# Kernel tuning notes

Hardware: AMD Instinct MI355X
Metric: run time of the kernel (lower is better)

## Reference

```python
import jax, jax.numpy as jnp
import numpy as np

ALPHA = 0.5
SMOOTH = 1e-05
ITERS = 10


def _max_pool3x3(x):
    # 3x3 max pool, stride 1, SAME padding on NCHW tensor
    return jax.lax.reduce_window(
        x, -jnp.inf, jax.lax.max,
        window_dimensions=(1, 1, 3, 3),
        window_strides=(1, 1, 1, 1),
        padding='SAME')


def _soft_erode(x):
    return -_max_pool3x3(-x)


def _soft_dilate(x):
    return _max_pool3x3(x)


def _soft_skeletonize(img, iterations=ITERS):
    def body(skel, _):
        eroded = _soft_erode(skel)
        temp = _soft_dilate(eroded)
        skel = skel - (skel - eroded) * temp
        skel = jnp.clip(skel, 0.0, 1.0)
        return skel, None
    skel, _ = jax.lax.scan(body, img, None, length=iterations)
    return skel


def _dice_score(pred, target, smooth=SMOOTH):
    inter = jnp.sum(pred * target, axis=(2, 3))
    union = jnp.sum(pred, axis=(2, 3)) + jnp.sum(target, axis=(2, 3))
    dice = (2.0 * inter + smooth) / (union + smooth)
    return jnp.mean(dice)


def setup_inputs() -> dict:
    key = jax.random.key(0)
    k1, k2 = jax.random.split(key)
    B, C, H, W = 32, 1, 512, 512
    pred_logits = jax.random.normal(k1, (B, C, H, W), dtype=jnp.float32)
    target = jax.random.uniform(k2, (B, C, H, W), dtype=jnp.float32)
    return {"pred_logits": pred_logits, "target": target}


def reference(pred_logits, target):
    pred = jax.nn.sigmoid(pred_logits)
    dice = _dice_score(pred, target)
    pred_skel = _soft_skeletonize(pred)
    target_skel = _soft_skeletonize(target)
    skel_dice = _dice_score(pred_skel, target_skel)
    loss = (1.0 - ALPHA) * (1.0 - dice) + ALPHA * (1.0 - skel_dice)
    return (loss, dice, skel_dice)
```

## Files before the change

### kernel.cpp

```cpp
#include <hip/hip_runtime.h>
#include <hip/hip_fp16.h>
#include <math.h>


#define H 512
#define W 512
#define IMG (H * W)
#define NIMG 64
#define NPRED 32

#define APU 72
#define AROWS 74
#define BPU 68
#define BROWS 68
#define TQ 17
#define S1ITEMS 238
#define FILLN (AROWS * 18)

#define PINF2 0x7C007C00u
#define NINF2 0xFC00FC00u
#define ONE2  0x3C003C00u

typedef _Float16 f16;
typedef _Float16 h2 __attribute__((ext_vector_type(2)));
typedef __fp16 fp16v2 __attribute__((ext_vector_type(2)));

__device__ __forceinline__ float2 unpack2(uint u) {
    fp16v2 h = __builtin_bit_cast(fp16v2, u);
    return make_float2((float)h.x, (float)h.y);
}
__device__ __forceinline__ uint pack2(float a, float b) {
    fp16v2 h = __builtin_amdgcn_cvt_pkrtz(a, b);
    return __builtin_bit_cast(uint, h);
}
__device__ __forceinline__ uint pmin(uint a, uint b) {
    uint d; asm("v_pk_min_f16 %0, %1, %2" : "=v"(d) : "v"(a), "v"(b)); return d;
}
__device__ __forceinline__ uint pmax(uint a, uint b) {
    uint d; asm("v_pk_max_f16 %0, %1, %2" : "=v"(d) : "v"(a), "v"(b)); return d;
}
__device__ __forceinline__ uint abit(uint hi, uint lo) {
    return __builtin_amdgcn_alignbit(hi, lo, 16);
}

__device__ __forceinline__ float wsum64(float v) {
#pragma unroll
    for (int o = 32; o > 0; o >>= 1) v += __shfl_down(v, o);
    return v;
}

__device__ __forceinline__ void hmin8p(const uint* __restrict__ p, uint m[6], uint sc[4]) {
    uint4 w0 = *(const uint4*)(p);
    uint4 w1 = *(const uint4*)(p + 4);
    uint w[8] = {w0.x, w0.y, w0.z, w0.w, w1.x, w1.y, w1.z, w1.w};
    sc[0] = w[2]; sc[1] = w[3]; sc[2] = w[4]; sc[3] = w[5];
    uint s[7];
#pragma unroll
    for (int j = 0; j < 7; j++) s[j] = abit(w[j + 1], w[j]);
#pragma unroll
    for (int i = 0; i < 6; i++) m[i] = pmin(s[i], pmin(w[i + 1], s[i + 1]));
}

template<bool EDGE>
__device__ __forceinline__ void erode8(const uint a[6], const uint b[6], const uint c[6],
                                       bool rowok, const bool* eok, uint e[6]) {
#pragma unroll
    for (int i = 0; i < 6; i++) {
        uint v = pmin(a[i], pmin(b[i], c[i]));
        e[i] = EDGE ? ((rowok && eok[i]) ? v : NINF2) : v;
    }
}

__device__ __forceinline__ void hmax8(const uint e[6], uint hx[4], uint ec[4]) {
    uint a[5];
#pragma unroll
    for (int j = 0; j < 5; j++) a[j] = abit(e[j + 1], e[j]);
#pragma unroll
    for (int p = 0; p < 4; p++) {
        hx[p] = pmax(a[p], pmax(e[p + 1], a[p + 1]));
        ec[p] = e[p + 1];
    }
}

__device__ __forceinline__ uint upd_pair(uint s, uint ec, uint t) {
    h2 sh = __builtin_bit_cast(h2, s);
    h2 eh = __builtin_bit_cast(h2, ec);
    h2 th = __builtin_bit_cast(h2, t);
    h2 o = sh - (sh - eh) * th;
    return pmin(pmax(__builtin_bit_cast(uint, o), 0u), ONE2);
}

template<bool EDGE, int SIG>
__device__ float2 fillA_f32(uint* __restrict__ A, const float* __restrict__ src,
                            const float* __restrict__ tgt,
                            int tileX, int tileY, int tid) {
    float a = 0.0f, b = 0.0f;
    for (int i = tid; i < FILLN; i += 256) {
        const int r = i / 18;
        const int q = i - 18 * r;
        const int gy = tileY + r - 4;
        const int gx = tileX - 8 + 8 * q;
        uint4 v = make_uint4(PINF2, PINF2, PINF2, PINF2);
        const bool ok = EDGE ? (r < 72 && (unsigned)gy < (unsigned)H &&
                                (unsigned)gx < (unsigned)W)
                             : true;
        if (ok) {
            const float* sp = src + (size_t)gy * W + gx;
            float4 f0 = *(const float4*)(sp);
            float4 f1 = *(const float4*)(sp + 4);
            if (SIG) {
                f0.x = 1.0f / (1.0f + __expf(-f0.x));
                f0.y = 1.0f / (1.0f + __expf(-f0.y));
                f0.z = 1.0f / (1.0f + __expf(-f0.z));
                f0.w = 1.0f / (1.0f + __expf(-f0.w));
                f1.x = 1.0f / (1.0f + __expf(-f1.x));
                f1.y = 1.0f / (1.0f + __expf(-f1.y));
                f1.z = 1.0f / (1.0f + __expf(-f1.z));
                f1.w = 1.0f / (1.0f + __expf(-f1.w));
            }
            if (((unsigned)(r - 4) < 64u) && ((unsigned)(q - 1) < 16u)) {
                if (SIG) {
                    const float* tp = tgt + (size_t)gy * W + gx;
                    float4 t0 = *(const float4*)(tp);
                    float4 t1 = *(const float4*)(tp + 4);
                    a += f0.x * t0.x + f0.y * t0.y + f0.z * t0.z + f0.w * t0.w
                       + f1.x * t1.x + f1.y * t1.y + f1.z * t1.z + f1.w * t1.w;
                    b += f0.x + f0.y + f0.z + f0.w + f1.x + f1.y + f1.z + f1.w;
                } else {
                    a += f0.x + f0.y + f0.z + f0.w + f1.x + f1.y + f1.z + f1.w;
                }
            }
            v.x = pack2(f0.x, f0.y); v.y = pack2(f0.z, f0.w);
            v.z = pack2(f1.x, f1.y); v.w = pack2(f1.z, f1.w);
        }
        *(uint4*)(A + r * APU + 4 * q) = v;
    }
    return make_float2(a, b);
}

template<bool EDGE>
__device__ void fillA_f16(uint* __restrict__ A, const f16* __restrict__ src,
                          int tileX, int tileY, int tid) {
    for (int i = tid; i < FILLN; i += 256) {
        const int r = i / 18;
        const int q = i - 18 * r;
        const int gy = tileY + r - 4;
        const int gx = tileX - 8 + 8 * q;
        uint4 v;
        if (EDGE) {
            v = make_uint4(PINF2, PINF2, PINF2, PINF2);
            if (r < 72 && (unsigned)gy < (unsigned)H && (unsigned)gx < (unsigned)W)
                v = *(const uint4*)(src + (size_t)gy * W + gx);
        } else {
            v = *(const uint4*)(src + (size_t)gy * W + gx);
        }
        *(uint4*)(A + r * APU + 4 * q) = v;
    }
}

template<bool EDGE>
__device__ void stage1(const uint* __restrict__ Au, uint* __restrict__ Bu,
                       int tileX, int tileY, int tid) {
    if (tid >= S1ITEMS) return;
    const int s = tid / TQ;
    const int g = tid - TQ * s;
    const int gcb = tileX + 8 * g - 4;
    const int ys = tileY - 2 + 5 * s;
    bool eok[6], wok[4];
    if (EDGE) {
#pragma unroll
        for (int i = 0; i < 6; i++) eok[i] = ((unsigned)(gcb - 2 + 2 * i) < (unsigned)W);
#pragma unroll
        for (int p = 0; p < 4; p++) wok[p] = ((unsigned)(gcb + 2 * p) < (unsigned)W);
    }
    const int lr = 5 * s + 2;
    const uint* Ab = Au + 4 * g;
    uint m[3][6], sc[3][4], hx[3][4], e[6], ec_cur[4], ec_nxt[4], tsc[4];
    hmin8p(Ab + (lr - 2) * APU, m[0], tsc);
    hmin8p(Ab + (lr - 1) * APU, m[1], tsc);
    hmin8p(Ab + (lr + 0) * APU, m[2], sc[0]);
    erode8<EDGE>(m[0], m[1], m[2], (unsigned)(ys - 1) < (unsigned)H, eok, e);
    hmax8(e, hx[0], ec_nxt);
    hmin8p(Ab + (lr + 1) * APU, m[0], sc[1]);
    erode8<EDGE>(m[1], m[2], m[0], (unsigned)ys < (unsigned)H, eok, e);
    hmax8(e, hx[1], ec_cur);
#pragma unroll
    for (int k = 0; k < 5; k++) {
        hmin8p(Ab + (lr + 2 + k) * APU, m[(k + 1) % 3], sc[(2 + k) % 3]);
        erode8<EDGE>(m[(k + 2) % 3], m[k % 3], m[(k + 1) % 3],
                     (unsigned)(ys + k + 1) < (unsigned)H, eok, e);
        hmax8(e, hx[(k + 2) % 3], ec_nxt);
        const int br = 5 * s + k;
        if (br < BROWS) {
            const bool rin = EDGE ? ((unsigned)(ys + k) < (unsigned)H) : true;
            uint o[4];
#pragma unroll
            for (int p = 0; p < 4; p++) {
                uint t = pmax(hx[k % 3][p], pmax(hx[(k + 1) % 3][p], hx[(k + 2) % 3][p]));
                uint v = upd_pair(sc[k % 3][p], ec_cur[p], t);
                o[p] = EDGE ? ((rin && wok[p]) ? v : PINF2) : v;
            }
            *(uint4*)(Bu + br * BPU + 4 * g) = make_uint4(o[0], o[1], o[2], o[3]);
        }
#pragma unroll
        for (int p = 0; p < 4; p++) ec_cur[p] = ec_nxt[p];
    }
}

template<bool EDGE, bool TOREG>
__device__ void stage2(const uint* __restrict__ Bu, int tileX, int tileY, int tid,
                       f16* __restrict__ gdst, uint* __restrict__ oreg) {
    const int g = tid & 15;
    const int ty = tid >> 4;
    const int X = tileX + 8 * g;
    const int gy0 = tileY + 4 * ty;
    const int rb = 4 * ty + 2;
    bool eok[6];
    if (EDGE) {
#pragma unroll
        for (int i = 0; i < 6; i++) eok[i] = ((unsigned)(X - 2 + 2 * i) < (unsigned)W);
    }
    const uint* Bb = Bu + 4 * g;
    uint m[3][6], sc[3][4], hx[3][4], e[6], ec_cur[4], ec_nxt[4], tsc[4];
    hmin8p(Bb + (rb - 2) * BPU, m[0], tsc);
    hmin8p(Bb + (rb - 1) * BPU, m[1], tsc);
    hmin8p(Bb + (rb + 0) * BPU, m[2], sc[0]);
    erode8<EDGE>(m[0], m[1], m[2], (unsigned)(gy0 - 1) < (unsigned)H, eok, e);
    hmax8(e, hx[0], ec_nxt);
    hmin8p(Bb + (rb + 1) * BPU, m[0], sc[1]);
    erode8<EDGE>(m[1], m[2], m[0], true, eok, e);
    hmax8(e, hx[1], ec_cur);
#pragma unroll
    for (int k = 0; k < 4; k++) {
        hmin8p(Bb + (rb + 2 + k) * BPU, m[(k + 1) % 3], sc[(2 + k) % 3]);
        erode8<EDGE>(m[(k + 2) % 3], m[k % 3], m[(k + 1) % 3],
                     (unsigned)(gy0 + k + 1) < (unsigned)H, eok, e);
        hmax8(e, hx[(k + 2) % 3], ec_nxt);
        uint o[4];
#pragma unroll
        for (int p = 0; p < 4; p++) {
            uint t = pmax(hx[k % 3][p], pmax(hx[(k + 1) % 3][p], hx[(k + 2) % 3][p]));
            o[p] = upd_pair(sc[k % 3][p], ec_cur[p], t);
        }
        if (TOREG) {
#pragma unroll
            for (int p = 0; p < 4; p++) oreg[4 * k + p] = o[p];
        } else {
            *(uint4*)(gdst + (size_t)(gy0 + k) * W + X) = make_uint4(o[0], o[1], o[2], o[3]);
        }
#pragma unroll
        for (int p = 0; p < 4; p++) ec_cur[p] = ec_nxt[p];
    }
}

__device__ __forceinline__ bool is_edge() {
    return (blockIdx.x == 0) | (blockIdx.x == 3) | (blockIdx.y == 0) | (blockIdx.y == 7);
}

__global__ __launch_bounds__(256, 4) void k_first(
    const float* __restrict__ logits, const float* __restrict__ target,
    f16* __restrict__ outb, float* __restrict__ parts0, float* __restrict__ parts1) {
    __shared__ __align__(16) uint A[AROWS * APU];
    __shared__ __align__(16) uint Bu[BROWS * BPU];
    __shared__ float red[8];
    const int img = blockIdx.z;
    const int tileX = blockIdx.x * 128, tileY = blockIdx.y * 64;
    const int tid = threadIdx.x;
    const bool pred = (img < NPRED);
    const bool edge = is_edge();
    float2 ab;
    if (edge) {
        if (pred) ab = fillA_f32<true, 1>(A, logits + (size_t)img * IMG,
                                          target + (size_t)img * IMG, tileX, tileY, tid);
        else      ab = fillA_f32<true, 0>(A, target + (size_t)(img - NPRED) * IMG,
                                          nullptr, tileX, tileY, tid);
    } else {
        if (pred) ab = fillA_f32<false, 1>(A, logits + (size_t)img * IMG,
                                           target + (size_t)img * IMG, tileX, tileY, tid);
        else      ab = fillA_f32<false, 0>(A, target + (size_t)(img - NPRED) * IMG,
                                           nullptr, tileX, tileY, tid);
    }
    __syncthreads();
    float a = wsum64(ab.x), b = wsum64(ab.y);
    if ((tid & 63) == 0) { red[tid >> 6] = a; red[4 + (tid >> 6)] = b; }
    if (edge) stage1<true>(A, Bu, tileX, tileY, tid);
    else      stage1<false>(A, Bu, tileX, tileY, tid);
    __syncthreads();
    if (tid == 0) {
        int bi = blockIdx.z * 32 + blockIdx.y * 4 + blockIdx.x;
        parts0[bi] = red[0] + red[1] + red[2] + red[3];
        parts1[bi] = red[4] + red[5] + red[6] + red[7];
    }
    if (edge) stage2<true, false>(Bu, tileX, tileY, tid, outb + (size_t)img * IMG, nullptr);
    else      stage2<false, false>(Bu, tileX, tileY, tid, outb + (size_t)img * IMG, nullptr);
}

__global__ __launch_bounds__(256, 4) void k_mid(
    const f16* __restrict__ in, f16* __restrict__ outb) {
    __shared__ __align__(16) uint A[AROWS * APU];
    __shared__ __align__(16) uint Bu[BROWS * BPU];
    const int img = blockIdx.z;
    const int tileX = blockIdx.x * 128, tileY = blockIdx.y * 64;
    const int tid = threadIdx.x;
    const bool edge = is_edge();
    if (edge) {
        fillA_f16<true>(A, in + (size_t)img * IMG, tileX, tileY, tid);
        __syncthreads();
        stage1<true>(A, Bu, tileX, tileY, tid);
        __syncthreads();
        stage2<true, false>(Bu, tileX, tileY, tid, outb + (size_t)img * IMG, nullptr);
    } else {
        fillA_f16<false>(A, in + (size_t)img * IMG, tileX, tileY, tid);
        __syncthreads();
        stage1<false>(A, Bu, tileX, tileY, tid);
        __syncthreads();
        stage2<false, false>(Bu, tileX, tileY, tid, outb + (size_t)img * IMG, nullptr);
    }
}

__global__ __launch_bounds__(256, 4) void k_last(
    const f16* __restrict__ in, float* __restrict__ pA,
    float* __restrict__ pB, float* __restrict__ pC) {
    __shared__ __align__(16) uint A[AROWS * APU];
    __shared__ __align__(16) uint Bu[BROWS * BPU];
    __shared__ float red[12];
    const int img = blockIdx.z;
    const int tileX = blockIdx.x * 128, tileY = blockIdx.y * 64;
    const int tid = threadIdx.x;
    const bool edge = is_edge();
    uint op[16], ot[16];
    if (edge) {
        fillA_f16<true>(A, in + (size_t)img * IMG, tileX, tileY, tid);
        __syncthreads();
        stage1<true>(A, Bu, tileX, tileY, tid);
        __syncthreads();
        stage2<true, true>(Bu, tileX, tileY, tid, nullptr, op);
        fillA_f16<true>(A, in + (size_t)(img + NPRED) * IMG, tileX, tileY, tid);
        __syncthreads();
        stage1<true>(A, Bu, tileX, tileY, tid);
        __syncthreads();
        stage2<true, true>(Bu, tileX, tileY, tid, nullptr, ot);
    } else {
        fillA_f16<false>(A, in + (size_t)img * IMG, tileX, tileY, tid);
        __syncthreads();
        stage1<false>(A, Bu, tileX, tileY, tid);
        __syncthreads();
        stage2<false, true>(Bu, tileX, tileY, tid, nullptr, op);
        fillA_f16<false>(A, in + (size_t)(img + NPRED) * IMG, tileX, tileY, tid);
        __syncthreads();
        stage1<false>(A, Bu, tileX, tileY, tid);
        __syncthreads();
        stage2<false, true>(Bu, tileX, tileY, tid, nullptr, ot);
    }
    float a = 0.0f, b = 0.0f, c = 0.0f;
#pragma unroll
    for (int j = 0; j < 16; j++) {
        float2 p = unpack2(op[j]);
        float2 t = unpack2(ot[j]);
        a += p.x * t.x + p.y * t.y;
        b += p.x + p.y;
        c += t.x + t.y;
    }
    a = wsum64(a); b = wsum64(b); c = wsum64(c);
    if ((tid & 63) == 0) {
        red[tid >> 6] = a; red[4 + (tid >> 6)] = b; red[8 + (tid >> 6)] = c;
    }
    __syncthreads();
    if (tid == 0) {
        int bi = img * 32 + blockIdx.y * 4 + blockIdx.x;
        pA[bi] = red[0] + red[1] + red[2] + red[3];
        pB[bi] = red[4] + red[5] + red[6] + red[7];
        pC[bi] = red[8] + red[9] + red[10] + red[11];
    }
}

__global__ __launch_bounds__(64) void finalize_img(
    const float* __restrict__ parts0, const float* __restrict__ parts1,
    const float* __restrict__ pA, const float* __restrict__ pB,
    const float* __restrict__ pC, float* __restrict__ dices) {
    const int i = blockIdx.x, t = threadIdx.x;
    const bool v = (t < 32);
    float inter = wsum64(v ? parts0[i * 32 + t] : 0.0f);
    float sp = wsum64(v ? parts1[i * 32 + t] : 0.0f);
    float st = wsum64(v ? parts0[(NPRED + i) * 32 + t] : 0.0f);
    float i2 = wsum64(v ? pA[i * 32 + t] : 0.0f);
    float sp2 = wsum64(v ? pB[i * 32 + t] : 0.0f);
    float st2 = wsum64(v ? pC[i * 32 + t] : 0.0f);
    if (t == 0) {
        dices[i] = (float)((2.0 * (double)inter + 1e-5) / ((double)sp + (double)st + 1e-5));
        dices[32 + i] = (float)((2.0 * (double)i2 + 1e-5) / ((double)sp2 + (double)st2 + 1e-5));
    }
}

__global__ void finalize_out(const float* __restrict__ dices, float* __restrict__ out) {
    const int t = threadIdx.x;
    double d = 0.0, sd = 0.0;
    if (t < 32) { d = dices[t]; sd = dices[32 + t]; }
#pragma unroll
    for (int o = 32; o > 0; o >>= 1) { d += __shfl_down(d, o); sd += __shfl_down(sd, o); }
    if (t == 0) {
        d *= (1.0 / 32.0); sd *= (1.0 / 32.0);
        out[0] = (float)(0.5 * (1.0 - d) + 0.5 * (1.0 - sd));
        out[1] = (float)d;
        out[2] = (float)sd;
    }
}

extern "C" void kernel_launch(void* const* d_in, const int* in_sizes, int n_in,
                              void* d_out, int out_size, void* d_ws, size_t ws_size,
                              hipStream_t stream) {
    (void)in_sizes; (void)n_in; (void)out_size; (void)ws_size;
    const float* logits = (const float*)d_in[0];
    const float* target = (const float*)d_in[1];
    float* out = (float*)d_out;
    f16* buf0 = (f16*)d_ws;
    f16* buf1 = buf0 + (size_t)NIMG * IMG;
    float* parts0 = (float*)(buf1 + (size_t)NIMG * IMG);
    float* parts1 = parts0 + 2048;
    float* pA = parts1 + 2048;
    float* pB = pA + 1024;
    float* pC = pB + 1024;
    float* dices = pC + 1024;

    dim3 blk(256, 1, 1);
    k_first<<<dim3(4, 8, NIMG), blk, 0, stream>>>(logits, target, buf0, parts0, parts1);
    k_mid<<<dim3(4, 8, NIMG), blk, 0, stream>>>(buf0, buf1);
    k_mid<<<dim3(4, 8, NIMG), blk, 0, stream>>>(buf1, buf0);
    k_mid<<<dim3(4, 8, NIMG), blk, 0, stream>>>(buf0, buf1);
    k_last<<<dim3(4, 8, NPRED), blk, 0, stream>>>(buf1, pA, pB, pC);
    finalize_img<<<32, 64, 0, stream>>>(parts0, parts1, pA, pB, pC, dices);
    finalize_out<<<1, 64, 0, stream>>>(dices, out);
}
```

Before: 227.6 us.

## Load fp16 tiles straight into LDS via global_load_lds and batch fp32 fill loads

The fp16 tile fill in the middle and last skeleton kernels now uses direct global-to-LDS loads (`global_load_lds`, 16 bytes per lane), so data no longer passes through VGPRs. Out-of-range rows are clamped to the nearest border row, which is equivalent for the min/max pooling, while out-of-range columns are still written as +inf. The fp32 first-pass fill is restructured to issue three iterations of loads before doing the sigmoid and dice math, exposing more memory-level parallelism. The gain in exchange is lower register pressure and load latency. The risks are relying on correct waitcnt handling before the barrier, and on the changed border semantics staying correct for the halo rows.

```diff
diff --git a/kernel.cpp b/kernel.cpp
--- a/kernel.cpp
+++ b/kernel.cpp
@@ -43,6 +43,12 @@
     return __builtin_amdgcn_alignbit(hi, lo, 16);
 }
 
+__device__ __forceinline__ void lds_dma16(uint* l, const void* g) {
+    __builtin_amdgcn_global_load_lds(
+        (__attribute__((address_space(1))) void*)(g),
+        (__attribute__((address_space(3))) void*)(l), 16, 0, 0);
+}
+
 __device__ __forceinline__ float wsum64(float v) {
 #pragma unroll
     for (int o = 32; o > 0; o >>= 1) v += __shfl_down(v, o);
@@ -95,66 +101,88 @@
                             const float* __restrict__ tgt,
                             int tileX, int tileY, int tid) {
     float a = 0.0f, b = 0.0f;
-    for (int i = tid; i < FILLN; i += 256) {
-        const int r = i / 18;
-        const int q = i - 18 * r;
-        const int gy = tileY + r - 4;
-        const int gx = tileX - 8 + 8 * q;
-        uint4 v = make_uint4(PINF2, PINF2, PINF2, PINF2);
-        const bool ok = EDGE ? (r < 72 && (unsigned)gy < (unsigned)H &&
-                                (unsigned)gx < (unsigned)W)
-                             : true;
-        if (ok) {
-            const float* sp = src + (size_t)gy * W + gx;
-            float4 f0 = *(const float4*)(sp);
-            float4 f1 = *(const float4*)(sp + 4);
-            if (SIG) {
-                f0.x = 1.0f / (1.0f + __expf(-f0.x));
-                f0.y = 1.0f / (1.0f + __expf(-f0.y));
-                f0.z = 1.0f / (1.0f + __expf(-f0.z));
-                f0.w = 1.0f / (1.0f + __expf(-f0.w));
-                f1.x = 1.0f / (1.0f + __expf(-f1.x));
-                f1.y = 1.0f / (1.0f + __expf(-f1.y));
-                f1.z = 1.0f / (1.0f + __expf(-f1.z));
-                f1.w = 1.0f / (1.0f + __expf(-f1.w));
-            }
-            if (((unsigned)(r - 4) < 64u) && ((unsigned)(q - 1) < 16u)) {
+#pragma unroll
+    for (int hf = 0; hf < 2; hf++) {
+        float4 v0[3], v1[3], t0[3], t1[3];
+        bool ld[3];
+#pragma unroll
+        for (int j = 0; j < 3; j++) {
+            const int i = tid + 256 * (3 * hf + j);
+            const int r = i / 18;
+            const int q = i - 18 * r;
+            const int gy = tileY + r - 4;
+            const int gx = tileX - 8 + 8 * q;
+            bool ok = (i < FILLN);
+            if (EDGE) ok = ok && (r < 72) && ((unsigned)gy < (unsigned)H) &&
+                           ((unsigned)gx < (unsigned)W);
+            ld[j] = ok;
+            if (ok) {
+                const float* sp = src + (size_t)gy * W + gx;
+                v0[j] = *(const float4*)(sp);
+                v1[j] = *(const float4*)(sp + 4);
                 if (SIG) {
                     const float* tp = tgt + (size_t)gy * W + gx;
-                    float4 t0 = *(const float4*)(tp);
-                    float4 t1 = *(const float4*)(tp + 4);
-                    a += f0.x * t0.x + f0.y * t0.y + f0.z * t0.z + f0.w * t0.w
-                       + f1.x * t1.x + f1.y * t1.y + f1.z * t1.z + f1.w * t1.w;
-                    b += f0.x + f0.y + f0.z + f0.w + f1.x + f1.y + f1.z + f1.w;
-                } else {
-                    a += f0.x + f0.y + f0.z + f0.w + f1.x + f1.y + f1.z + f1.w;
+                    t0[j] = *(const float4*)(tp);
+                    t1[j] = *(const float4*)(tp + 4);
                 }
             }
-            v.x = pack2(f0.x, f0.y); v.y = pack2(f0.z, f0.w);
-            v.z = pack2(f1.x, f1.y); v.w = pack2(f1.z, f1.w);
-        }
-        *(uint4*)(A + r * APU + 4 * q) = v;
+        }
+#pragma unroll
+        for (int j = 0; j < 3; j++) {
+            const int i = tid + 256 * (3 * hf + j);
+            const int r = i / 18;
+            const int q = i - 18 * r;
+            if (i < FILLN) {
+                uint4 w = make_uint4(PINF2, PINF2, PINF2, PINF2);
+                if (ld[j]) {
+                    float4 f0 = v0[j], f1 = v1[j];
+                    if (SIG) {
+                        f0.x = 1.0f / (1.0f + __expf(-f0.x));
+                        f0.y = 1.0f / (1.0f + __expf(-f0.y));
+                        f0.z = 1.0f / (1.0f + __expf(-f0.z));
+                        f0.w = 1.0f / (1.0f + __expf(-f0.w));
+                        f1.x = 1.0f / (1.0f + __expf(-f1.x));
+                        f1.y = 1.0f / (1.0f + __expf(-f1.y));
+                        f1.z = 1.0f / (1.0f + __expf(-f1.z));
+                        f1.w = 1.0f / (1.0f + __expf(-f1.w));
+                    }
+                    if (((unsigned)(r - 4) < 64u) && ((unsigned)(q - 1) < 16u)) {
+                        if (SIG) {
+                            a += f0.x * t0[j].x + f0.y * t0[j].y + f0.z * t0[j].z +
+                                 f0.w * t0[j].w + f1.x * t1[j].x + f1.y * t1[j].y +
+                                 f1.z * t1[j].z + f1.w * t1[j].w;
+                            b += f0.x + f0.y + f0.z + f0.w + f1.x + f1.y + f1.z + f1.w;
+                        } else {
+                            a += f0.x + f0.y + f0.z + f0.w + f1.x + f1.y + f1.z + f1.w;
+                        }
+                    }
+                    w.x = pack2(f0.x, f0.y); w.y = pack2(f0.z, f0.w);
+                    w.z = pack2(f1.x, f1.y); w.w = pack2(f1.z, f1.w);
+                }
+                *(uint4*)(A + r * APU + 4 * q) = w;
+            }
+        }
     }
     return make_float2(a, b);
 }
 
-template<bool EDGE>
-__device__ void fillA_f16(uint* __restrict__ A, const f16* __restrict__ src,
-                          int tileX, int tileY, int tid) {
-    for (int i = tid; i < FILLN; i += 256) {
-        const int r = i / 18;
-        const int q = i - 18 * r;
-        const int gy = tileY + r - 4;
-        const int gx = tileX - 8 + 8 * q;
-        uint4 v;
-        if (EDGE) {
-            v = make_uint4(PINF2, PINF2, PINF2, PINF2);
-            if (r < 72 && (unsigned)gy < (unsigned)H && (unsigned)gx < (unsigned)W)
-                v = *(const uint4*)(src + (size_t)gy * W + gx);
-        } else {
-            v = *(const uint4*)(src + (size_t)gy * W + gx);
-        }
-        *(uint4*)(A + r * APU + 4 * q) = v;
+__device__ __forceinline__ void fill_dma(uint* __restrict__ A, const f16* __restrict__ src,
+                                         int tileX, int tileY, int tid) {
+#pragma unroll
+    for (int j = 0; j < 6; j++) {
+        const int i = tid + 256 * j;
+        if (i < FILLN) {
+            const int r = i / 18;
+            const int q = i - 18 * r;
+            const int gy = tileY + r - 4;
+            const int gx = tileX - 8 + 8 * q;
+            if (gx < 0 || gx >= W) {
+                *(uint4*)(A + 4 * i) = make_uint4(PINF2, PINF2, PINF2, PINF2);
+            } else {
+                const int gyc = min(max(gy, 0), H - 1);
+                lds_dma16(A + 4 * i, src + (size_t)gyc * W + gx);
+            }
+        }
     }
 }
 
@@ -303,15 +331,13 @@
     const int tileX = blockIdx.x * 128, tileY = blockIdx.y * 64;
     const int tid = threadIdx.x;
     const bool edge = is_edge();
+    fill_dma(A, in + (size_t)img * IMG, tileX, tileY, tid);
+    __syncthreads();
     if (edge) {
-        fillA_f16<true>(A, in + (size_t)img * IMG, tileX, tileY, tid);
-        __syncthreads();
         stage1<true>(A, Bu, tileX, tileY, tid);
         __syncthreads();
         stage2<true, false>(Bu, tileX, tileY, tid, outb + (size_t)img * IMG, nullptr);
     } else {
-        fillA_f16<false>(A, in + (size_t)img * IMG, tileX, tileY, tid);
-        __syncthreads();
         stage1<false>(A, Bu, tileX, tileY, tid);
         __syncthreads();
         stage2<false, false>(Bu, tileX, tileY, tid, outb + (size_t)img * IMG, nullptr);
@@ -329,24 +355,22 @@
     const int tid = threadIdx.x;
     const bool edge = is_edge();
     uint op[16], ot[16];
+    fill_dma(A, in + (size_t)img * IMG, tileX, tileY, tid);
+    __syncthreads();
     if (edge) {
-        fillA_f16<true>(A, in + (size_t)img * IMG, tileX, tileY, tid);
-        __syncthreads();
         stage1<true>(A, Bu, tileX, tileY, tid);
         __syncthreads();
         stage2<true, true>(Bu, tileX, tileY, tid, nullptr, op);
-        fillA_f16<true>(A, in + (size_t)(img + NPRED) * IMG, tileX, tileY, tid);
+        fill_dma(A, in + (size_t)(img + NPRED) * IMG, tileX, tileY, tid);
         __syncthreads();
         stage1<true>(A, Bu, tileX, tileY, tid);
         __syncthreads();
         stage2<true, true>(Bu, tileX, tileY, tid, nullptr, ot);
     } else {
-        fillA_f16<false>(A, in + (size_t)img * IMG, tileX, tileY, tid);
-        __syncthreads();
         stage1<false>(A, Bu, tileX, tileY, tid);
         __syncthreads();
         stage2<false, true>(Bu, tileX, tileY, tid, nullptr, op);
-        fillA_f16<false>(A, in + (size_t)(img + NPRED) * IMG, tileX, tileY, tid);
+        fill_dma(A, in + (size_t)(img + NPRED) * IMG, tileX, tileY, tid);
         __syncthreads();
         stage1<false>(A, Bu, tileX, tileY, tid);
         __syncthreads();
```

Measured after the change: 220.0 us. 1.03x faster.
